# Kernel tuning notes

Hardware: AMD Instinct MI355X
Metric: run time of the kernel (lower is better)

Reference implementation:

```python
import jax, jax.numpy as jnp
import numpy as np

N_NODES = 100000
N_EDGES = 1600000
IN_DIM, HID_DIM, OUT_DIM = 128, 64, 128


def setup_inputs() -> dict:
    key = jax.random.key(0)
    k1, k2, k3, k4 = jax.random.split(key, 4)
    x = jax.random.normal(k1, (N_NODES, IN_DIM), dtype=jnp.float32)
    edge_index = jax.random.randint(k2, (2, N_EDGES), 0, N_NODES, dtype=jnp.int32)
    W_conv = jax.random.normal(k3, (IN_DIM, HID_DIM), dtype=jnp.float32) * (1.0 / np.sqrt(IN_DIM))
    b_conv = jnp.zeros((HID_DIM,), dtype=jnp.float32)
    W_lin = jax.random.normal(k4, (HID_DIM, OUT_DIM), dtype=jnp.float32) * (1.0 / np.sqrt(HID_DIM))
    b_lin = jnp.zeros((OUT_DIM,), dtype=jnp.float32)
    return {"x": x, "edge_index": edge_index, "W_conv": W_conv, "b_conv": b_conv,
            "W_lin": W_lin, "b_lin": b_lin}


def gcn_conv(x, edge_index, W, b):
    """PyG GCNConv: linear transform, symmetric-normalized aggregation with self-loops, bias."""
    n = x.shape[0]
    loop = jnp.arange(n, dtype=edge_index.dtype)
    src = jnp.concatenate([edge_index[0], loop])  # message sources (x_j)
    dst = jnp.concatenate([edge_index[1], loop])  # aggregation targets
    # degree of target nodes (counting self-loops), D^{-1/2}
    deg = jax.ops.segment_sum(jnp.ones_like(dst, dtype=x.dtype), dst, num_segments=n)
    dinv = jnp.where(deg > 0, jax.lax.rsqrt(deg), 0.0)
    norm = dinv[src] * dinv[dst]  # [E+N]
    h = x @ W  # [N, hid]
    msg = h[src] * norm[:, None]  # gather + normalize, [E+N, hid]
    agg = jax.ops.segment_sum(msg, dst, num_segments=n)  # scatter-add
    return agg + b


def reference(x, edge_index, W_conv, b_conv, W_lin, b_lin):
    h = gcn_conv(x, edge_index, W_conv, b_conv)
    h = jax.nn.relu(h)
    return h @ W_lin + b_lin
```

## Files before the change

### kernel.cpp

```cpp
#include <hip/hip_runtime.h>
#include <hip/hip_bf16.h>

#define NN 100000
#define NE 1600000
#define NBUK 782
#define NBLK 400
#define CHUNK 4000
#define NGB 1563

typedef unsigned short ushort_t;
typedef __bf16 bf16x8 __attribute__((ext_vector_type(8)));
typedef float  f32x4  __attribute__((ext_vector_type(4)));

static __device__ __forceinline__ float bf2f(ushort_t u) {
    union { unsigned int i; float f; } c; c.i = ((unsigned int)u) << 16; return c.f;
}
static __device__ __forceinline__ ushort_t f2bf(float f) {
    union { __hip_bfloat16 b; ushort_t u; } c; c.b = __float2bfloat16(f); return c.u;
}

__global__ __launch_bounds__(256) void k_part_hist(const int* __restrict__ dst,
                                                   int* __restrict__ bhist) {
    __shared__ int h[NBUK];
    int t = threadIdx.x, b = blockIdx.x;
    for (int i = t; i < NBUK; i += 256) h[i] = 0;
    __syncthreads();
    int e0 = b * CHUNK;
    for (int r = 0; r < CHUNK; r += 256)
        if (r + t < CHUNK) atomicAdd(&h[dst[e0 + r + t] >> 7], 1);
    __syncthreads();
    for (int i = t; i < NBUK; i += 256) bhist[b * NBUK + i] = h[i];
}

__global__ __launch_bounds__(512) void k_colscan(const int* __restrict__ bhist,
                                                 int* __restrict__ base_excl,
                                                 int* __restrict__ coltot) {
    __shared__ int s[512];
    int k = blockIdx.x, t = threadIdx.x;
    int v = (t < NBLK) ? bhist[t * NBUK + k] : 0;
    s[t] = v;
    __syncthreads();
#pragma unroll
    for (int o = 1; o < 512; o <<= 1) {
        int x = (t >= o) ? s[t - o] : 0;
        __syncthreads();
        s[t] += x;
        __syncthreads();
    }
    if (t < NBLK) base_excl[t * NBUK + k] = s[t] - v;
    if (t == 511) coltot[k] = s[511];
}

__global__ __launch_bounds__(1024) void k_scanb2(const int* __restrict__ coltot,
                                                 int* __restrict__ bstart,
                                                 int* __restrict__ bcnt) {
    __shared__ int s[1024];
    int t = threadIdx.x;
    int v = (t < NBUK) ? coltot[t] : 0;
    s[t] = v;
    __syncthreads();
#pragma unroll
    for (int o = 1; o < 1024; o <<= 1) {
        int x = (t >= o) ? s[t - o] : 0;
        __syncthreads();
        s[t] += x;
        __syncthreads();
    }
    if (t < NBUK) { bstart[t] = s[t] - v; bcnt[t] = v; }
}

__global__ __launch_bounds__(256) void k_scatter2(const int* __restrict__ ei,
                                                  const int* __restrict__ bstart,
                                                  const int* __restrict__ base_excl,
                                                  unsigned* __restrict__ ebuf) {
    __shared__ int cur[NBUK];
    int t = threadIdx.x, b = blockIdx.x;
    for (int i = t; i < NBUK; i += 256) cur[i] = 0;
    __syncthreads();
    int e0 = b * CHUNK;
    for (int r = 0; r < CHUNK; r += 256) {
        if (r + t < CHUNK) {
            int e = e0 + r + t;
            int sv = ei[e];
            int dv = ei[NE + e];
            int k = dv >> 7;
            int rk = atomicAdd(&cur[k], 1);
            int pos = bstart[k] + base_excl[b * NBUK + k] + rk;
            ebuf[pos] = (unsigned)sv | ((unsigned)(dv & 127) << 17);
        }
    }
}

__global__ __launch_bounds__(256) void k_sort(const int* __restrict__ bstart,
                                              const int* __restrict__ bcnt,
                                              const unsigned* __restrict__ ebuf,
                                              int* __restrict__ csr,
                                              int* __restrict__ offsets,
                                              int* __restrict__ deg,
                                              float* __restrict__ dinv) {
    __shared__ int hist[128];
    __shared__ int off[128];
    __shared__ int cur[128];
    int t = threadIdx.x, b = blockIdx.x;
    if (t < 128) hist[t] = 0;
    __syncthreads();
    int base = bstart[b], ne = bcnt[b];
    for (int i = t; i < ne; i += 256) atomicAdd(&hist[ebuf[base + i] >> 17], 1);
    __syncthreads();
    if (t < 128) off[t] = hist[t];
    __syncthreads();
#pragma unroll
    for (int o = 1; o < 128; o <<= 1) {
        int x = 0;
        if (t < 128 && t >= o) x = off[t - o];
        __syncthreads();
        if (t < 128) off[t] += x;
        __syncthreads();
    }
    if (t < 128) {
        int excl = off[t] - hist[t];
        cur[t] = excl;
        int node = b * 128 + t;
        if (node < NN) {
            offsets[node] = base + excl;
            deg[node]     = hist[t];
            dinv[node]    = rsqrtf((float)(hist[t] + 1));
        }
    }
    __syncthreads();
    for (int i = t; i < ne; i += 256) {
        unsigned pe = ebuf[base + i];
        int dl = pe >> 17;
        int pos = atomicAdd(&cur[dl], 1);
        csr[base + pos] = (int)(pe & 0x1FFFF);
    }
}

__global__ __launch_bounds__(256) void k_gemm1(const float* __restrict__ x,
                                               const float* __restrict__ Wf,
                                               const float* __restrict__ dinv,
                                               ushort_t* __restrict__ hp) {
    __shared__ __align__(16) ushort_t xs[64 * 136];
    __shared__ __align__(16) ushort_t wt[64 * 136];
    __shared__ float dv[64];
    int t = threadIdx.x;
    int node0 = blockIdx.x * 64;

#pragma unroll 1
    for (int r = 0; r < 32; ++r) {
        int i = r * 256 + t;
        int k = i >> 6, d = i & 63;
        wt[d * 136 + k] = f2bf(Wf[i]);
    }
#pragma unroll 1
    for (int r = 0; r < 8; ++r) {
        int i4 = r * 256 + t;
        int flat = i4 * 4;
        int nl = flat >> 7, k = flat & 127;
        int gn = node0 + nl; gn = gn < NN ? gn : NN - 1;
        float4 v = *(const float4*)(x + (size_t)gn * 128 + k);
        unsigned u0 = (unsigned)f2bf(v.x) | ((unsigned)f2bf(v.y) << 16);
        unsigned u1 = (unsigned)f2bf(v.z) | ((unsigned)f2bf(v.w) << 16);
        uint2 p; p.x = u0; p.y = u1;
        *(uint2*)&xs[nl * 136 + k] = p;
    }
    if (t < 64) { int gn = node0 + t; dv[t] = dinv[gn < NN ? gn : NN - 1]; }
    __syncthreads();

    int w = t >> 6, lane = t & 63;
    int l15 = lane & 15, quad = lane >> 4;
    f32x4 acc[4];
#pragma unroll
    for (int ct = 0; ct < 4; ++ct) { acc[ct][0]=0.f; acc[ct][1]=0.f; acc[ct][2]=0.f; acc[ct][3]=0.f; }

#pragma unroll
    for (int kt = 0; kt < 4; ++kt) {
        bf16x8 av = *(const bf16x8*)&xs[(w * 16 + l15) * 136 + kt * 32 + quad * 8];
#pragma unroll
        for (int ct = 0; ct < 4; ++ct) {
            bf16x8 bv = *(const bf16x8*)&wt[(ct * 16 + l15) * 136 + kt * 32 + quad * 8];
            acc[ct] = __builtin_amdgcn_mfma_f32_16x16x32_bf16(av, bv, acc[ct], 0, 0, 0);
        }
    }
#pragma unroll
    for (int reg = 0; reg < 4; ++reg) {
        int nl = w * 16 + quad * 4 + reg;
        int gn = node0 + nl;
        if (gn < NN) {
            float dvv = dv[nl];
#pragma unroll
            for (int ct = 0; ct < 4; ++ct)
                hp[(size_t)gn * 64 + ct * 16 + l15] = f2bf(dvv * acc[ct][reg]);
        }
    }
}

__global__ __launch_bounds__(256) void k_gather(const int* __restrict__ offsets,
                                                const int* __restrict__ deg,
                                                const int* __restrict__ csr,
                                                const float* __restrict__ dinv,
                                                const ushort_t* __restrict__ hp,
                                                const float* __restrict__ b_conv,
                                                ushort_t* __restrict__ a) {
    int node = (blockIdx.x * 256 + threadIdx.x) >> 6;
    int lane = threadIdx.x & 63;
    int start = offsets[node];
    int cnt   = deg[node];

    float s0 = 0.f, s1 = 0.f, s2 = 0.f, s3 = 0.f;
#pragma unroll 1
    for (int j0 = 0; j0 < cnt; j0 += 64) {
        int m = cnt - j0; m = m < 64 ? m : 64;
        int col = 0;
        if (lane < m) col = csr[start + j0 + lane];
        int jj = 0;
#pragma unroll 1
        for (; jj + 8 <= m; jj += 8) {
            int c[8];
#pragma unroll
            for (int u = 0; u < 8; ++u) c[u] = __shfl(col, jj + u, 64);
            float v[8];
#pragma unroll
            for (int u = 0; u < 8; ++u) v[u] = bf2f(hp[(size_t)c[u] * 64 + lane]);
            s0 += v[0] + v[4]; s1 += v[1] + v[5]; s2 += v[2] + v[6]; s3 += v[3] + v[7];
        }
        for (; jj < m; ++jj) {
            int c = __shfl(col, jj, 64);
            s0 += bf2f(hp[(size_t)c * 64 + lane]);
        }
    }
    float acc = (s0 + s1) + (s2 + s3);
    acc += bf2f(hp[(size_t)node * 64 + lane]);
    float v = dinv[node] * acc + b_conv[lane];
    a[(size_t)node * 64 + lane] = f2bf(fmaxf(v, 0.f));
}

__global__ __launch_bounds__(256) void k_epi(const ushort_t* __restrict__ a,
                                             const float* __restrict__ W2f,
                                             const float* __restrict__ blin,
                                             float* __restrict__ out) {
    __shared__ __align__(16) ushort_t as[64 * 72];
    __shared__ __align__(16) ushort_t w2t[128 * 72];
    __shared__ float bl[128];
    int t = threadIdx.x;
    int node0 = blockIdx.x * 64;

#pragma unroll
    for (int r = 0; r < 2; ++r) {
        int i8 = r * 256 + t;
        int flat = i8 * 8;
        int nl = flat >> 6, k = flat & 63;
        int gn = node0 + nl; gn = gn < NN ? gn : NN - 1;
        uint4 v = *(const uint4*)(a + (size_t)gn * 64 + k);
        *(uint4*)&as[nl * 72 + k] = v;
    }
#pragma unroll 1
    for (int r = 0; r < 32; ++r) {
        int i = r * 256 + t;
        int k = i >> 7, j = i & 127;
        w2t[j * 72 + k] = f2bf(W2f[i]);
    }
    if (t < 128) bl[t] = blin[t];
    __syncthreads();

    int w = t >> 6, lane = t & 63;
    int l15 = lane & 15, quad = lane >> 4;
    f32x4 acc[8];
#pragma unroll
    for (int ct = 0; ct < 8; ++ct) { acc[ct][0]=0.f; acc[ct][1]=0.f; acc[ct][2]=0.f; acc[ct][3]=0.f; }

#pragma unroll
    for (int kt = 0; kt < 2; ++kt) {
        bf16x8 av = *(const bf16x8*)&as[(w * 16 + l15) * 72 + kt * 32 + quad * 8];
#pragma unroll
        for (int ct = 0; ct < 8; ++ct) {
            bf16x8 bv = *(const bf16x8*)&w2t[(ct * 16 + l15) * 72 + kt * 32 + quad * 8];
            acc[ct] = __builtin_amdgcn_mfma_f32_16x16x32_bf16(av, bv, acc[ct], 0, 0, 0);
        }
    }
#pragma unroll
    for (int reg = 0; reg < 4; ++reg) {
        int nl = w * 16 + quad * 4 + reg;
        int gn = node0 + nl;
        if (gn < NN) {
#pragma unroll
            for (int ct = 0; ct < 8; ++ct) {
                int j = ct * 16 + l15;
                out[(size_t)gn * 128 + j] = acc[ct][reg] + bl[j];
            }
        }
    }
}

extern "C" void kernel_launch(void* const* d_in, const int* in_sizes, int n_in,
                              void* d_out, int out_size, void* d_ws, size_t ws_size,
                              hipStream_t stream) {
    const float* x  = (const float*)d_in[0];
    const int*   ei = (const int*)d_in[1];
    const float* Wc = (const float*)d_in[2];
    const float* bc = (const float*)d_in[3];
    const float* Wl = (const float*)d_in[4];
    const float* bl = (const float*)d_in[5];
    float* out = (float*)d_out;

    char* ws = (char*)d_ws;
    int*      bhist     = (int*)(ws + 0);
    int*      base_excl = (int*)(ws + 1251200);
    int*      coltot    = (int*)(ws + 2502400);
    int*      bstart    = (int*)(ws + 2505600);
    int*      bcnt      = (int*)(ws + 2508800);
    int*      offsets   = (int*)(ws + 2512000);
    int*      deg       = (int*)(ws + 2912384);
    float*    dinv      = (float*)(ws + 3312768);
    unsigned* ebuf      = (unsigned*)(ws + 3713152);
    int*      csr       = (int*)(ws + 10113152);
    ushort_t* hp        = (ushort_t*)(ws + 16513152);
    ushort_t* a         = (ushort_t*)(ws + 29313152);

    k_part_hist<<<NBLK, 256, 0, stream>>>(ei + NE, bhist);
    k_colscan <<<NBUK, 512, 0, stream>>>(bhist, base_excl, coltot);
    k_scanb2  <<<1, 1024, 0, stream>>>(coltot, bstart, bcnt);
    k_scatter2<<<NBLK, 256, 0, stream>>>(ei, bstart, base_excl, ebuf);
    k_sort    <<<NBUK, 256, 0, stream>>>(bstart, bcnt, ebuf, csr, offsets, deg, dinv);
    k_gemm1   <<<NGB, 256, 0, stream>>>(x, Wc, dinv, hp);
    k_gather  <<<NN * 64 / 256, 256, 0, stream>>>(offsets, deg, csr, dinv, hp, bc, a);
    k_epi     <<<NGB, 256, 0, stream>>>(a, Wl, bl, out);
}
```

Baseline: 252.6 us.

## Pre-convert weights once, drop LDS staging in GEMMs, vectorize gather loads

A new small kernel converts both weight matrices to transposed bf16 once, reusing the ebuf workspace region after the sort has finished with it. The two GEMM kernels then drop their shared-memory staging and read x/a and the weights straight from global memory into MFMA operands, with the operand roles swapped so that output stores become vectorized. The gather kernel now has each 16-lane group fetch 8-byte chunks from four neighbor rows at once, then reduces across groups with xor shuffles. This cuts per-block weight conversion and scalar 2-byte gathers, at the cost of more redundant global weight reads and masked out-of-range loads.

```diff
diff --git a/kernel.cpp b/kernel.cpp
--- a/kernel.cpp
+++ b/kernel.cpp
@@ -12,8 +12,11 @@
 typedef __bf16 bf16x8 __attribute__((ext_vector_type(8)));
 typedef float  f32x4  __attribute__((ext_vector_type(4)));
 
-static __device__ __forceinline__ float bf2f(ushort_t u) {
-    union { unsigned int i; float f; } c; c.i = ((unsigned int)u) << 16; return c.f;
+static __device__ __forceinline__ float bf2f(unsigned u) {
+    union { unsigned i; float f; } c; c.i = u << 16; return c.f;
+}
+static __device__ __forceinline__ float bf2f_hi(unsigned u) {
+    union { unsigned i; float f; } c; c.i = u & 0xffff0000u; return c.f;
 }
 static __device__ __forceinline__ ushort_t f2bf(float f) {
     union { __hip_bfloat16 b; ushort_t u; } c; c.b = __float2bfloat16(f); return c.u;
@@ -136,61 +139,53 @@
     }
 }
 
+__global__ __launch_bounds__(256) void k_wprep(const float* __restrict__ Wc,
+                                               const float* __restrict__ Wl,
+                                               ushort_t* __restrict__ wtb,
+                                               ushort_t* __restrict__ w2tb) {
+    int t = blockIdx.x * 256 + threadIdx.x;
+    int d = t & 63, k = t >> 6;
+    wtb[d * 128 + k] = f2bf(Wc[t]);
+    int j = t & 127, k2 = t >> 7;
+    w2tb[j * 64 + k2] = f2bf(Wl[t]);
+}
+
 __global__ __launch_bounds__(256) void k_gemm1(const float* __restrict__ x,
-                                               const float* __restrict__ Wf,
+                                               const ushort_t* __restrict__ wtb,
                                                const float* __restrict__ dinv,
                                                ushort_t* __restrict__ hp) {
-    __shared__ __align__(16) ushort_t xs[64 * 136];
-    __shared__ __align__(16) ushort_t wt[64 * 136];
-    __shared__ float dv[64];
     int t = threadIdx.x;
-    int node0 = blockIdx.x * 64;
-
-#pragma unroll 1
-    for (int r = 0; r < 32; ++r) {
-        int i = r * 256 + t;
-        int k = i >> 6, d = i & 63;
-        wt[d * 136 + k] = f2bf(Wf[i]);
-    }
-#pragma unroll 1
-    for (int r = 0; r < 8; ++r) {
-        int i4 = r * 256 + t;
-        int flat = i4 * 4;
-        int nl = flat >> 7, k = flat & 127;
-        int gn = node0 + nl; gn = gn < NN ? gn : NN - 1;
-        float4 v = *(const float4*)(x + (size_t)gn * 128 + k);
-        unsigned u0 = (unsigned)f2bf(v.x) | ((unsigned)f2bf(v.y) << 16);
-        unsigned u1 = (unsigned)f2bf(v.z) | ((unsigned)f2bf(v.w) << 16);
-        uint2 p; p.x = u0; p.y = u1;
-        *(uint2*)&xs[nl * 136 + k] = p;
-    }
-    if (t < 64) { int gn = node0 + t; dv[t] = dinv[gn < NN ? gn : NN - 1]; }
-    __syncthreads();
-
-    int w = t >> 6, lane = t & 63;
-    int l15 = lane & 15, quad = lane >> 4;
+    int w = t >> 6, lane = t & 63, l15 = lane & 15, quad = lane >> 4;
+    int gn = blockIdx.x * 64 + w * 16 + l15;
+    int gnc = gn < NN ? gn : NN - 1;
+    const float*    xp = x   + (size_t)gnc * 128 + quad * 8;
+    const ushort_t* wp = wtb + l15 * 128 + quad * 8;
     f32x4 acc[4];
 #pragma unroll
-    for (int ct = 0; ct < 4; ++ct) { acc[ct][0]=0.f; acc[ct][1]=0.f; acc[ct][2]=0.f; acc[ct][3]=0.f; }
+    for (int dt = 0; dt < 4; ++dt) { acc[dt][0]=0.f; acc[dt][1]=0.f; acc[dt][2]=0.f; acc[dt][3]=0.f; }
 
 #pragma unroll
     for (int kt = 0; kt < 4; ++kt) {
-        bf16x8 av = *(const bf16x8*)&xs[(w * 16 + l15) * 136 + kt * 32 + quad * 8];
-#pragma unroll
-        for (int ct = 0; ct < 4; ++ct) {
-            bf16x8 bv = *(const bf16x8*)&wt[(ct * 16 + l15) * 136 + kt * 32 + quad * 8];
-            acc[ct] = __builtin_amdgcn_mfma_f32_16x16x32_bf16(av, bv, acc[ct], 0, 0, 0);
-        }
-    }
-#pragma unroll
-    for (int reg = 0; reg < 4; ++reg) {
-        int nl = w * 16 + quad * 4 + reg;
-        int gn = node0 + nl;
-        if (gn < NN) {
-            float dvv = dv[nl];
-#pragma unroll
-            for (int ct = 0; ct < 4; ++ct)
-                hp[(size_t)gn * 64 + ct * 16 + l15] = f2bf(dvv * acc[ct][reg]);
+        float4 v0 = *(const float4*)(xp + kt * 32);
+        float4 v1 = *(const float4*)(xp + kt * 32 + 4);
+        union { ushort_t u[8]; bf16x8 v; } cv;
+        cv.u[0]=f2bf(v0.x); cv.u[1]=f2bf(v0.y); cv.u[2]=f2bf(v0.z); cv.u[3]=f2bf(v0.w);
+        cv.u[4]=f2bf(v1.x); cv.u[5]=f2bf(v1.y); cv.u[6]=f2bf(v1.z); cv.u[7]=f2bf(v1.w);
+        bf16x8 bv = cv.v;
+#pragma unroll
+        for (int dt = 0; dt < 4; ++dt) {
+            bf16x8 av = *(const bf16x8*)(wp + dt * 16 * 128 + kt * 32);
+            acc[dt] = __builtin_amdgcn_mfma_f32_16x16x32_bf16(av, bv, acc[dt], 0, 0, 0);
+        }
+    }
+    if (gn < NN) {
+        float dv = dinv[gn];
+#pragma unroll
+        for (int dt = 0; dt < 4; ++dt) {
+            uint2 o;
+            o.x = (unsigned)f2bf(dv * acc[dt][0]) | ((unsigned)f2bf(dv * acc[dt][1]) << 16);
+            o.y = (unsigned)f2bf(dv * acc[dt][2]) | ((unsigned)f2bf(dv * acc[dt][3]) << 16);
+            *(uint2*)&hp[(size_t)gn * 64 + dt * 16 + quad * 4] = o;
         }
     }
 }
@@ -202,10 +197,13 @@
                                                 const ushort_t* __restrict__ hp,
                                                 const float* __restrict__ b_conv,
                                                 ushort_t* __restrict__ a) {
-    int node = (blockIdx.x * 256 + threadIdx.x) >> 6;
+    int node = __builtin_amdgcn_readfirstlane((blockIdx.x * 256 + threadIdx.x) >> 6);
     int lane = threadIdx.x & 63;
+    int g   = lane >> 4;
+    int l16 = lane & 15;
     int start = offsets[node];
     int cnt   = deg[node];
+    const ushort_t* hpc = hp + l16 * 4;
 
     float s0 = 0.f, s1 = 0.f, s2 = 0.f, s3 = 0.f;
 #pragma unroll 1
@@ -213,81 +211,84 @@
         int m = cnt - j0; m = m < 64 ? m : 64;
         int col = 0;
         if (lane < m) col = csr[start + j0 + lane];
-        int jj = 0;
-#pragma unroll 1
-        for (; jj + 8 <= m; jj += 8) {
-            int c[8];
-#pragma unroll
-            for (int u = 0; u < 8; ++u) c[u] = __shfl(col, jj + u, 64);
-            float v[8];
-#pragma unroll
-            for (int u = 0; u < 8; ++u) v[u] = bf2f(hp[(size_t)c[u] * 64 + lane]);
-            s0 += v[0] + v[4]; s1 += v[1] + v[5]; s2 += v[2] + v[6]; s3 += v[3] + v[7];
-        }
-        for (; jj < m; ++jj) {
-            int c = __shfl(col, jj, 64);
-            s0 += bf2f(hp[(size_t)c * 64 + lane]);
-        }
-    }
-    float acc = (s0 + s1) + (s2 + s3);
-    acc += bf2f(hp[(size_t)node * 64 + lane]);
-    float v = dinv[node] * acc + b_conv[lane];
-    a[(size_t)node * 64 + lane] = f2bf(fmaxf(v, 0.f));
+#pragma unroll 2
+        for (int jj = 0; jj < m; jj += 16) {
+            int e0 = jj + g, e1 = jj + 4 + g, e2 = jj + 8 + g, e3 = jj + 12 + g;
+            int c0 = __shfl(col, e0, 64);
+            int c1 = __shfl(col, e1, 64);
+            int c2 = __shfl(col, e2, 64);
+            int c3 = __shfl(col, e3, 64);
+            uint2 d0 = *(const uint2*)(hpc + (size_t)c0 * 64);
+            uint2 d1 = *(const uint2*)(hpc + (size_t)c1 * 64);
+            uint2 d2 = *(const uint2*)(hpc + (size_t)c2 * 64);
+            uint2 d3 = *(const uint2*)(hpc + (size_t)c3 * 64);
+            if (e0 >= m) { d0.x = 0u; d0.y = 0u; }
+            if (e1 >= m) { d1.x = 0u; d1.y = 0u; }
+            if (e2 >= m) { d2.x = 0u; d2.y = 0u; }
+            if (e3 >= m) { d3.x = 0u; d3.y = 0u; }
+            s0 += bf2f(d0.x);    s1 += bf2f_hi(d0.x);
+            s2 += bf2f(d0.y);    s3 += bf2f_hi(d0.y);
+            s0 += bf2f(d1.x);    s1 += bf2f_hi(d1.x);
+            s2 += bf2f(d1.y);    s3 += bf2f_hi(d1.y);
+            s0 += bf2f(d2.x);    s1 += bf2f_hi(d2.x);
+            s2 += bf2f(d2.y);    s3 += bf2f_hi(d2.y);
+            s0 += bf2f(d3.x);    s1 += bf2f_hi(d3.x);
+            s2 += bf2f(d3.y);    s3 += bf2f_hi(d3.y);
+        }
+    }
+    s0 += __shfl_xor(s0, 16, 64); s1 += __shfl_xor(s1, 16, 64);
+    s2 += __shfl_xor(s2, 16, 64); s3 += __shfl_xor(s3, 16, 64);
+    s0 += __shfl_xor(s0, 32, 64); s1 += __shfl_xor(s1, 32, 64);
+    s2 += __shfl_xor(s2, 32, 64); s3 += __shfl_xor(s3, 32, 64);
+
+    uint2 sl = *(const uint2*)(hpc + (size_t)node * 64);
+    s0 += bf2f(sl.x); s1 += bf2f_hi(sl.x); s2 += bf2f(sl.y); s3 += bf2f_hi(sl.y);
+    float dv = dinv[node];
+    float4 bc = *(const float4*)(b_conv + l16 * 4);
+    float v0 = fmaxf(dv * s0 + bc.x, 0.f);
+    float v1 = fmaxf(dv * s1 + bc.y, 0.f);
+    float v2 = fmaxf(dv * s2 + bc.z, 0.f);
+    float v3 = fmaxf(dv * s3 + bc.w, 0.f);
+    if (lane < 16) {
+        uint2 o;
+        o.x = (unsigned)f2bf(v0) | ((unsigned)f2bf(v1) << 16);
+        o.y = (unsigned)f2bf(v2) | ((unsigned)f2bf(v3) << 16);
+        *(uint2*)&a[(size_t)node * 64 + l16 * 4] = o;
+    }
 }
 
 __global__ __launch_bounds__(256) void k_epi(const ushort_t* __restrict__ a,
-                                             const float* __restrict__ W2f,
+                                             const ushort_t* __restrict__ w2tb,
                                              const float* __restrict__ blin,
                                              float* __restrict__ out) {
-    __shared__ __align__(16) ushort_t as[64 * 72];
-    __shared__ __align__(16) ushort_t w2t[128 * 72];
-    __shared__ float bl[128];
     int t = threadIdx.x;
-    int node0 = blockIdx.x * 64;
-
-#pragma unroll
-    for (int r = 0; r < 2; ++r) {
-        int i8 = r * 256 + t;
-        int flat = i8 * 8;
-        int nl = flat >> 6, k = flat & 63;
-        int gn = node0 + nl; gn = gn < NN ? gn : NN - 1;
-        uint4 v = *(const uint4*)(a + (size_t)gn * 64 + k);
-        *(uint4*)&as[nl * 72 + k] = v;
-    }
-#pragma unroll 1
-    for (int r = 0; r < 32; ++r) {
-        int i = r * 256 + t;
-        int k = i >> 7, j = i & 127;
-        w2t[j * 72 + k] = f2bf(W2f[i]);
-    }
-    if (t < 128) bl[t] = blin[t];
-    __syncthreads();
-
-    int w = t >> 6, lane = t & 63;
-    int l15 = lane & 15, quad = lane >> 4;
+    int w = t >> 6, lane = t & 63, l15 = lane & 15, quad = lane >> 4;
+    int gn = blockIdx.x * 64 + w * 16 + l15;
+    int gnc = gn < NN ? gn : NN - 1;
+    const ushort_t* ap = a    + (size_t)gnc * 64 + quad * 8;
+    const ushort_t* wp = w2tb + l15 * 64 + quad * 8;
     f32x4 acc[8];
 #pragma unroll
-    for (int ct = 0; ct < 8; ++ct) { acc[ct][0]=0.f; acc[ct][1]=0.f; acc[ct][2]=0.f; acc[ct][3]=0.f; }
+    for (int jt = 0; jt < 8; ++jt) { acc[jt][0]=0.f; acc[jt][1]=0.f; acc[jt][2]=0.f; acc[jt][3]=0.f; }
 
 #pragma unroll
     for (int kt = 0; kt < 2; ++kt) {
-        bf16x8 av = *(const bf16x8*)&as[(w * 16 + l15) * 72 + kt * 32 + quad * 8];
-#pragma unroll
-        for (int ct = 0; ct < 8; ++ct) {
-            bf16x8 bv = *(const bf16x8*)&w2t[(ct * 16 + l15) * 72 + kt * 32 + quad * 8];
-            acc[ct] = __builtin_amdgcn_mfma_f32_16x16x32_bf16(av, bv, acc[ct], 0, 0, 0);
-        }
-    }
-#pragma unroll
-    for (int reg = 0; reg < 4; ++reg) {
-        int nl = w * 16 + quad * 4 + reg;
-        int gn = node0 + nl;
-        if (gn < NN) {
-#pragma unroll
-            for (int ct = 0; ct < 8; ++ct) {
-                int j = ct * 16 + l15;
-                out[(size_t)gn * 128 + j] = acc[ct][reg] + bl[j];
-            }
+        bf16x8 bv = *(const bf16x8*)(ap + kt * 32);
+#pragma unroll
+        for (int jt = 0; jt < 8; ++jt) {
+            bf16x8 av = *(const bf16x8*)(wp + jt * 16 * 64 + kt * 32);
+            acc[jt] = __builtin_amdgcn_mfma_f32_16x16x32_bf16(av, bv, acc[jt], 0, 0, 0);
+        }
+    }
+    if (gn < NN) {
+#pragma unroll
+        for (int jt = 0; jt < 8; ++jt) {
+            int j0 = jt * 16 + quad * 4;
+            float4 b4 = *(const float4*)(blin + j0);
+            float4 o;
+            o.x = acc[jt][0] + b4.x; o.y = acc[jt][1] + b4.y;
+            o.z = acc[jt][2] + b4.z; o.w = acc[jt][3] + b4.w;
+            *(float4*)&out[(size_t)gn * 128 + j0] = o;
         }
     }
 }
@@ -316,13 +317,16 @@
     int*      csr       = (int*)(ws + 10113152);
     ushort_t* hp        = (ushort_t*)(ws + 16513152);
     ushort_t* a         = (ushort_t*)(ws + 29313152);
+    ushort_t* wtb  = (ushort_t*)(ws + 3713152);
+    ushort_t* w2tb = wtb + 8192;
 
     k_part_hist<<<NBLK, 256, 0, stream>>>(ei + NE, bhist);
     k_colscan <<<NBUK, 512, 0, stream>>>(bhist, base_excl, coltot);
     k_scanb2  <<<1, 1024, 0, stream>>>(coltot, bstart, bcnt);
     k_scatter2<<<NBLK, 256, 0, stream>>>(ei, bstart, base_excl, ebuf);
     k_sort    <<<NBUK, 256, 0, stream>>>(bstart, bcnt, ebuf, csr, offsets, deg, dinv);
-    k_gemm1   <<<NGB, 256, 0, stream>>>(x, Wc, dinv, hp);
+    k_wprep   <<<32, 256, 0, stream>>>(Wc, Wl, wtb, w2tb);
+    k_gemm1   <<<NGB, 256, 0, stream>>>(x, wtb, dinv, hp);
     k_gather  <<<NN * 64 / 256, 256, 0, stream>>>(offsets, deg, csr, dinv, hp, bc, a);
-    k_epi     <<<NGB, 256, 0, stream>>>(a, Wl, bl, out);
-}
+    k_epi     <<<NGB, 256, 0, stream>>>(a, w2tb, bl, out);
+}
```

After: 235.6 us. -6.7%, faster.
